# Optimization experiments

Hardware: AMD Instinct MI355X
Metric: run time of the kernel (lower is better)

Reference implementation:

```python
import jax, jax.numpy as jnp
import numpy as np

NUM_USERS, NUM_ITEMS, NUM_GROUPS = 100000, 50000, 20000
D = 64
B, M = 16384, 50


def setup_inputs() -> dict:
    key = jax.random.key(0)
    ks = jax.random.split(key, 16)
    inp = {
        "group_inputs": jax.random.randint(ks[0], (B,), 0, NUM_GROUPS),
        "item_inputs": jax.random.randint(ks[1], (B,), 0, NUM_ITEMS),
        "member_ids": jax.random.randint(ks[2], (B, M), 0, NUM_USERS),
        "member_lengths": jax.random.randint(ks[3], (B,), 0, M),
        # embedding tables (xavier-ish scale)
        "user_table": jax.random.normal(ks[4], (NUM_USERS, D), jnp.float32) * 0.05,
        "item_table": jax.random.normal(ks[5], (NUM_ITEMS, D), jnp.float32) * 0.05,
        "group_table": jax.random.normal(ks[6], (NUM_GROUPS, D), jnp.float32) * 0.05,
        # attention MLP: 2D -> 16 -> 1
        "att_w1": jax.random.normal(ks[7], (2 * D, 16), jnp.float32) * 0.1,
        "att_b1": jnp.zeros((16,), jnp.float32),
        "att_w2": jax.random.normal(ks[8], (16, 1), jnp.float32) * 0.1,
        "att_b2": jnp.zeros((1,), jnp.float32),
        # predict MLP: 3D -> 8 -> 1
        "pred_w1": jax.random.normal(ks[9], (3 * D, 8), jnp.float32) * 0.1,
        "pred_b1": jnp.zeros((8,), jnp.float32),
        "pred_w2": jax.random.normal(ks[10], (8, 1), jnp.float32) * 0.1,
        "pred_b2": jnp.zeros((1,), jnp.float32),
    }
    return inp


def reference(group_inputs, item_inputs, member_ids, member_lengths,
              user_table, item_table, group_table,
              att_w1, att_b1, att_w2, att_b2,
              pred_w1, pred_b1, pred_w2, pred_b2):
    # mask: at least one valid member per group
    mask = jnp.arange(M)[None, :] <= member_lengths[:, None]          # [B, M] bool
    mem_e = user_table[member_ids]                                    # [B, M, D]
    item_e = item_table[item_inputs]                                  # [B, D]

    # attention over members: concat(member, item) -> 16 -> 1
    gi = jnp.concatenate(
        [mem_e, jnp.broadcast_to(item_e[:, None, :], mem_e.shape)], axis=-1)  # [B, M, 2D]
    h = jax.nn.relu(jnp.einsum('bmk,kh->bmh', gi, att_w1) + att_b1)   # [B, M, 16]
    scores = (jnp.einsum('bmh,ho->bmo', h, att_w2) + att_b2)[..., 0]  # [B, M]
    scores = jnp.where(mask, scores, -jnp.inf)
    at_wt = jax.nn.softmax(scores, axis=-1)                           # [B, M]

    g_att = jnp.einsum('bm,bmd->bd', at_wt, mem_e)                    # [B, D]
    g = g_att + group_table[group_inputs]                             # [B, D]

    elem = g * item_e
    new_e = jnp.concatenate([elem, g, item_e], axis=-1)               # [B, 3D]
    ph = jax.nn.relu(new_e @ pred_w1 + pred_b1)                       # [B, 8]
    y = jax.nn.sigmoid(ph @ pred_w2 + pred_b2)                        # [B, 1]
    return y
```

## Files before the change

### kernel.cpp

```cpp
#include <hip/hip_runtime.h>
#include <math.h>

constexpr int MM = 50;
constexpr int DD = 64;
constexpr int HH = 16;
constexpr int PH = 8;
constexpr int ROWSTRIDE = DD + 1;
constexpr int WAVES_PER_BLOCK = 4;

__global__ __launch_bounds__(256) void agree_kernel(
    const int* __restrict__ group_inputs,
    const int* __restrict__ item_inputs,
    const int* __restrict__ member_ids,
    const int* __restrict__ member_lengths,
    const float* __restrict__ user_table,
    const float* __restrict__ item_table,
    const float* __restrict__ group_table,
    const float* __restrict__ att_w1,
    const float* __restrict__ att_b1,
    const float* __restrict__ att_w2,
    const float* __restrict__ att_b2,
    const float* __restrict__ pred_w1,
    const float* __restrict__ pred_b1,
    const float* __restrict__ pred_w2,
    const float* __restrict__ pred_b2,
    float* __restrict__ out,
    int B)
{
    __shared__ float lds_mem[WAVES_PER_BLOCK][MM * ROWSTRIDE];
    __shared__ float lds_wt[WAVES_PER_BLOCK][64];

    const int lane = threadIdx.x & 63;
    const int wave = threadIdx.x >> 6;
    const int b = blockIdx.x * WAVES_PER_BLOCK + wave;
    if (b >= B) return;

    const int* ids = member_ids + b * MM;
    float* tile = &lds_mem[wave][0];
    #pragma unroll 5
    for (int r = 0; r < MM; ++r) {
        const int id = ids[r];
        tile[r * ROWSTRIDE + lane] = user_table[(size_t)id * DD + lane];
    }

    const int item_idx = item_inputs[b];
    const float item_d = item_table[(size_t)item_idx * DD + lane];

    float h[HH];
    {
        const float* w1row = att_w1 + (size_t)(DD + lane) * HH;
        #pragma unroll
        for (int j = 0; j < HH; ++j) h[j] = item_d * w1row[j];
        #pragma unroll
        for (int off = 32; off > 0; off >>= 1) {
            #pragma unroll
            for (int j = 0; j < HH; ++j) h[j] += __shfl_xor(h[j], off, 64);
        }
        #pragma unroll
        for (int j = 0; j < HH; ++j) h[j] += att_b1[j];
    }

    const int len = member_lengths[b];
    const int mrow = (lane < MM) ? lane : 0;
    const float* myrow = tile + mrow * ROWSTRIDE;

    #pragma unroll 4
    for (int d = 0; d < DD; ++d) {
        const float x = myrow[d];
        const float* w1d = att_w1 + (size_t)d * HH;
        #pragma unroll
        for (int j = 0; j < HH; ++j) h[j] = fmaf(x, w1d[j], h[j]);
    }

    float score = att_b2[0];
    #pragma unroll
    for (int j = 0; j < HH; ++j) score = fmaf(fmaxf(h[j], 0.0f), att_w2[j], score);

    const bool valid = (lane < MM) && (lane <= len);
    score = valid ? score : -INFINITY;

    float mx = score;
    #pragma unroll
    for (int off = 32; off > 0; off >>= 1) mx = fmaxf(mx, __shfl_xor(mx, off, 64));
    float e = valid ? __expf(score - mx) : 0.0f;
    float sum = e;
    #pragma unroll
    for (int off = 32; off > 0; off >>= 1) sum += __shfl_xor(sum, off, 64);
    lds_wt[wave][lane] = e / sum;

    float g = 0.0f;
    #pragma unroll 5
    for (int m = 0; m < MM; ++m) {
        g = fmaf(lds_wt[wave][m], tile[m * ROWSTRIDE + lane], g);
    }
    const int gid = group_inputs[b];
    g += group_table[(size_t)gid * DD + lane];

    const float elem = g * item_d;
    float p[PH];
    {
        const float* pa = pred_w1 + (size_t)lane * PH;
        const float* pb = pred_w1 + (size_t)(DD + lane) * PH;
        const float* pc = pred_w1 + (size_t)(2 * DD + lane) * PH;
        #pragma unroll
        for (int j = 0; j < PH; ++j)
            p[j] = fmaf(elem, pa[j], fmaf(g, pb[j], item_d * pc[j]));
    }
    #pragma unroll
    for (int off = 32; off > 0; off >>= 1) {
        #pragma unroll
        for (int j = 0; j < PH; ++j) p[j] += __shfl_xor(p[j], off, 64);
    }

    if (lane == 0) {
        float acc = pred_b2[0];
        #pragma unroll
        for (int j = 0; j < PH; ++j)
            acc = fmaf(fmaxf(p[j] + pred_b1[j], 0.0f), pred_w2[j], acc);
        out[b] = 1.0f / (1.0f + __expf(-acc));
    }
}

extern "C" void kernel_launch(void* const* d_in, const int* in_sizes, int n_in,
                              void* d_out, int out_size, void* d_ws, size_t ws_size,
                              hipStream_t stream) {
    const int*   group_inputs   = (const int*)d_in[0];
    const int*   item_inputs    = (const int*)d_in[1];
    const int*   member_ids     = (const int*)d_in[2];
    const int*   member_lengths = (const int*)d_in[3];
    const float* user_table     = (const float*)d_in[4];
    const float* item_table     = (const float*)d_in[5];
    const float* group_table    = (const float*)d_in[6];
    const float* att_w1         = (const float*)d_in[7];
    const float* att_b1         = (const float*)d_in[8];
    const float* att_w2         = (const float*)d_in[9];
    const float* att_b2         = (const float*)d_in[10];
    const float* pred_w1        = (const float*)d_in[11];
    const float* pred_b1        = (const float*)d_in[12];
    const float* pred_w2        = (const float*)d_in[13];
    const float* pred_b2        = (const float*)d_in[14];
    float* out = (float*)d_out;

    const int B = in_sizes[0];
    const int blocks = (B + WAVES_PER_BLOCK - 1) / WAVES_PER_BLOCK;
    agree_kernel<<<blocks, 256, 0, stream>>>(
        group_inputs, item_inputs, member_ids, member_lengths,
        user_table, item_table, group_table,
        att_w1, att_b1, att_w2, att_b2,
        pred_w1, pred_b1, pred_w2, pred_b2,
        out, B);
}
```

Measured before the change: 174.8 us.

## Drop LDS member tile; read embeddings directly and skip masked members

Removes the per-wave LDS staging of all 50 member rows. Each lane now reads its own member row from global memory with float4 loads to compute the attention scores. The weighted sum re-gathers only the valid members (up to len+1), using member ids and weights kept in LDS. This cuts LDS footprint, which should raise occupancy, and skips the masked tail rows. The cost is a second global read of the valid member rows and uncoalesced per-lane row reads in the score phase. A raw s_waitcnt replaces an explicit barrier for the intra-wave LDS handoff.

```diff
diff --git a/kernel.cpp b/kernel.cpp
--- a/kernel.cpp
+++ b/kernel.cpp
@@ -5,7 +5,6 @@
 constexpr int DD = 64;
 constexpr int HH = 16;
 constexpr int PH = 8;
-constexpr int ROWSTRIDE = DD + 1;
 constexpr int WAVES_PER_BLOCK = 4;
 
 __global__ __launch_bounds__(256) void agree_kernel(
@@ -27,21 +26,17 @@
     float* __restrict__ out,
     int B)
 {
-    __shared__ float lds_mem[WAVES_PER_BLOCK][MM * ROWSTRIDE];
-    __shared__ float lds_wt[WAVES_PER_BLOCK][64];
+    __shared__ float lds_wt[WAVES_PER_BLOCK][MM];
+    __shared__ int   lds_id[WAVES_PER_BLOCK][MM];
 
     const int lane = threadIdx.x & 63;
     const int wave = threadIdx.x >> 6;
     const int b = blockIdx.x * WAVES_PER_BLOCK + wave;
     if (b >= B) return;
 
-    const int* ids = member_ids + b * MM;
-    float* tile = &lds_mem[wave][0];
-    #pragma unroll 5
-    for (int r = 0; r < MM; ++r) {
-        const int id = ids[r];
-        tile[r * ROWSTRIDE + lane] = user_table[(size_t)id * DD + lane];
-    }
+    const int my_m = (lane < MM) ? lane : (MM - 1);
+    const int my_id = member_ids[b * MM + my_m];
+    if (lane < MM) lds_id[wave][lane] = my_id;
 
     const int item_idx = item_inputs[b];
     const float item_d = item_table[(size_t)item_idx * DD + lane];
@@ -60,22 +55,25 @@
         for (int j = 0; j < HH; ++j) h[j] += att_b1[j];
     }
 
-    const int len = member_lengths[b];
-    const int mrow = (lane < MM) ? lane : 0;
-    const float* myrow = tile + mrow * ROWSTRIDE;
-
+    const float* myrow = user_table + (size_t)my_id * DD;
     #pragma unroll 4
-    for (int d = 0; d < DD; ++d) {
-        const float x = myrow[d];
-        const float* w1d = att_w1 + (size_t)d * HH;
+    for (int d4 = 0; d4 < DD / 4; ++d4) {
+        const float4 x = ((const float4*)myrow)[d4];
+        const float* w1d = att_w1 + (size_t)(d4 * 4) * HH;
         #pragma unroll
-        for (int j = 0; j < HH; ++j) h[j] = fmaf(x, w1d[j], h[j]);
+        for (int j = 0; j < HH; ++j) {
+            h[j] = fmaf(x.x, w1d[0 * HH + j], h[j]);
+            h[j] = fmaf(x.y, w1d[1 * HH + j], h[j]);
+            h[j] = fmaf(x.z, w1d[2 * HH + j], h[j]);
+            h[j] = fmaf(x.w, w1d[3 * HH + j], h[j]);
+        }
     }
 
     float score = att_b2[0];
     #pragma unroll
     for (int j = 0; j < HH; ++j) score = fmaf(fmaxf(h[j], 0.0f), att_w2[j], score);
 
+    const int len = member_lengths[b];
     const bool valid = (lane < MM) && (lane <= len);
     score = valid ? score : -INFINITY;
 
@@ -86,12 +84,16 @@
     float sum = e;
     #pragma unroll
     for (int off = 32; off > 0; off >>= 1) sum += __shfl_xor(sum, off, 64);
-    lds_wt[wave][lane] = e / sum;
+    if (lane < MM) lds_wt[wave][lane] = e / sum;
+    __builtin_amdgcn_s_waitcnt(0);
 
+    const int mcnt = (len < MM - 1 ? len : MM - 1) + 1;
     float g = 0.0f;
-    #pragma unroll 5
-    for (int m = 0; m < MM; ++m) {
-        g = fmaf(lds_wt[wave][m], tile[m * ROWSTRIDE + lane], g);
+    #pragma unroll 2
+    for (int m = 0; m < mcnt; ++m) {
+        const float wm  = lds_wt[wave][m];
+        const int   idm = lds_id[wave][m];
+        g = fmaf(wm, user_table[(size_t)idm * DD + lane], g);
     }
     const int gid = group_inputs[b];
     g += group_table[(size_t)gid * DD + lane];
```

New measurement: 158.9 us. 1.1x faster.
